# Performance work log

Hardware: AMD Instinct MI355X
Metric: run time of the kernel (lower is better)

Reference implementation:

```python
import jax, jax.numpy as jnp
import numpy as np

N_NODES = 50000
N_EDGES = 400000
N_GRAPHS = 64
EMB = 64
H = 128
EPS = 1e-5


def _prelu(x, a):
    return jnp.where(x > 0, x, a * x)


def _batchnorm(x, gamma, beta):
    mu = x.mean(0)
    var = x.var(0)
    return gamma * (x - mu) * jax.lax.rsqrt(var + EPS) + beta


def _sage_layer(xs, W_self, W_neigh, b, a, gamma, beta, src, dst):
    # xs: list of 3 [N, Din]; params stacked over the 3 relations
    outs = []
    for i in range(3):
        x = xs[i]
        msg = x[src[i]]                                   # [E, Din] neighbor gather
        nsum = jax.ops.segment_sum(msg, dst[i], num_segments=N_NODES)
        deg = jax.ops.segment_sum(jnp.ones((src.shape[1], 1), x.dtype), dst[i], num_segments=N_NODES)
        nmean = nsum / jnp.maximum(deg, 1.0)              # zero-degree -> 0 (DGL mean reduce)
        out = x @ W_self[i] + nmean @ W_neigh[i] + b[i]
        out = _prelu(out, a[i])                           # PReLU(h_feats)
        out = _batchnorm(out, gamma[i], beta[i])          # BatchNorm1d over nodes
        outs.append(out)
    return outs


def setup_inputs() -> dict:
    key = jax.random.key(0)
    ks = jax.random.split(key, 24)
    f32 = jnp.float32
    s = 0.05
    inp = {
        'h_idx': jax.random.randint(ks[0], (N_NODES,), 0, 257),
        'p_idx': jax.random.randint(ks[1], (N_NODES,), 0, 257),
        'hp_idx': jax.random.randint(ks[2], (N_NODES,), 0, 257),
        'src': jax.random.randint(ks[3], (3, N_EDGES), 0, N_NODES),
        'dst': jax.random.randint(ks[4], (3, N_EDGES), 0, N_NODES),
        'seg': jnp.sort(jax.random.randint(ks[5], (3, N_NODES), 0, N_GRAPHS), axis=1),
        'emb_h': jax.random.normal(ks[6], (257, EMB), f32) * s,
        'emb_p': jax.random.normal(ks[7], (257, EMB), f32) * s,
        'emb_hp': jax.random.normal(ks[8], (257, EMB), f32) * s,
        # layer 1 (in = EMB)
        'W1_self': jax.random.normal(ks[9], (3, EMB, H), f32) * s,
        'W1_neigh': jax.random.normal(ks[10], (3, EMB, H), f32) * s,
        'b1': jnp.zeros((3, H), f32),
        'a1': jnp.full((3, H), 0.25, f32),
        'gamma1': jnp.ones((3, H), f32),
        'beta1': jnp.zeros((3, H), f32),
        # layers 2-4 (in = H)
        'W_self': jax.random.normal(ks[11], (3, 3, H, H), f32) * s,
        'W_neigh': jax.random.normal(ks[12], (3, 3, H, H), f32) * s,
        'b': jnp.zeros((3, 3, H), f32),
        'a': jnp.full((3, 3, H), 0.25, f32),
        'gamma': jnp.ones((3, 3, H), f32),
        'beta': jnp.zeros((3, 3, H), f32),
    }
    return inp


def reference(h_idx, p_idx, hp_idx, src, dst, seg,
              emb_h, emb_p, emb_hp,
              W1_self, W1_neigh, b1, a1, gamma1, beta1,
              W_self, W_neigh, b, a, gamma, beta):
    xs = [emb_h[h_idx], emb_p[p_idx], emb_hp[hp_idx]]      # embedding lookups
    h1 = _sage_layer(xs, W1_self, W1_neigh, b1, a1, gamma1, beta1, src, dst)
    h2 = _sage_layer(h1, W_self[0], W_neigh[0], b[0], a[0], gamma[0], beta[0], src, dst)
    h3 = _sage_layer(h2, W_self[1], W_neigh[1], b[1], a[1], gamma[1], beta[1], src, dst)
    h4 = _sage_layer(h3, W_self[2], W_neigh[2], b[2], a[2], gamma[2], beta[2], src, dst)
    vecs = []
    for i in range(3):
        hcat = jnp.concatenate((h1[i], h2[i], h3[i], h4[i]), axis=1)   # [N, 4H]
        gsum = jax.ops.segment_sum(hcat, seg[i], num_segments=N_GRAPHS)
        cnt = jax.ops.segment_sum(jnp.ones((N_NODES, 1), hcat.dtype), seg[i], num_segments=N_GRAPHS)
        vecs.append(gsum / jnp.maximum(cnt, 1.0))                      # mean_nodes
    return jnp.concatenate(vecs, axis=1)                               # [B, 12H]
```

## Files before the change

kernel.cpp:

```cpp
#include <hip/hip_runtime.h>

#define N_NODES 50000
#define N_EDGES 400000
#define N_GRAPHS 64
#define EMB 64
#define H 128
#define EPS 1e-5f

#define NCHD 8
#define CHD 6250
#define NSLICE 48

typedef __attribute__((ext_vector_type(8))) short bf16x8;
typedef __attribute__((ext_vector_type(4))) float f32x4;

__device__ __forceinline__ unsigned short f2b(float f) {
    unsigned int u = __builtin_bit_cast(unsigned int, f);
    unsigned int r = (u + 0x7fff + ((u >> 16) & 1)) >> 16;
    return (unsigned short)r;
}


__global__ void count_deg_kernel(const int* __restrict__ dst, int* __restrict__ deg) {
    int rel = blockIdx.y;
    int e = blockIdx.x * 256 + threadIdx.x;
    if (e < N_EDGES) atomicAdd(&deg[rel * N_NODES + dst[rel * N_EDGES + e]], 1);
}

__global__ void scan_kernel(const int* __restrict__ deg, int* __restrict__ row_ptr,
                            int* __restrict__ cur) {
    int rel = blockIdx.x;
    const int* d = deg + rel * N_NODES;
    int* rp = row_ptr + rel * (N_NODES + 1);
    int* cu = cur + rel * N_NODES;
    __shared__ int sm[1024];
    __shared__ int carry;
    if (threadIdx.x == 0) carry = 0;
    __syncthreads();
    for (int base = 0; base < N_NODES; base += 4096) {
        int i0 = base + (int)threadIdx.x * 4;
        int v[4];
        int s = 0;
#pragma unroll
        for (int k = 0; k < 4; k++) { v[k] = (i0 + k < N_NODES) ? d[i0 + k] : 0; s += v[k]; }
        sm[threadIdx.x] = s;
        __syncthreads();
        for (int off = 1; off < 1024; off <<= 1) {
            int t = (threadIdx.x >= off) ? sm[threadIdx.x - off] : 0;
            __syncthreads();
            sm[threadIdx.x] += t;
            __syncthreads();
        }
        int run = carry + sm[threadIdx.x] - s;
#pragma unroll
        for (int k = 0; k < 4; k++) {
            if (i0 + k < N_NODES) { rp[i0 + k] = run; cu[i0 + k] = run; }
            run += v[k];
        }
        __syncthreads();
        if (threadIdx.x == 1023) carry += sm[1023];
        __syncthreads();
    }
    if (threadIdx.x == 0) rp[N_NODES] = carry;
}

__global__ void fill_part_kernel(const int* __restrict__ src, const int* __restrict__ dst,
                                 int* __restrict__ cur, int* __restrict__ edge_src) {
    int rel = blockIdx.z;
    int lo = blockIdx.y * CHD, hi = lo + CHD;
    const int* ds = dst + (size_t)rel * N_EDGES;
    const int* ss = src + (size_t)rel * N_EDGES;
    int* cu = cur + rel * N_NODES;
    int* es = edge_src + (size_t)rel * N_EDGES;
    for (int e = blockIdx.x * 256 + threadIdx.x; e < N_EDGES; e += NSLICE * 256) {
        int dn = ds[e];
        if (dn >= lo && dn < hi) {
            int pos = atomicAdd(&cu[dn], 1);
            es[pos] = ss[e];
        }
    }
}

__global__ void sort_adj_kernel(const int* __restrict__ row_ptr, int* __restrict__ edge_src) {
    int i = blockIdx.x * 256 + threadIdx.x;
    if (i >= 3 * N_NODES) return;
    int rel = i / N_NODES, n = i - rel * N_NODES;
    const int* rp = row_ptr + rel * (N_NODES + 1);
    int* es = edge_src + rel * N_EDGES;
    int s0 = rp[n], s1 = rp[n + 1];
    for (int a = s0 + 1; a < s1; a++) {
        int key = es[a];
        int b = a - 1;
        while (b >= s0 && es[b] > key) { es[b + 1] = es[b]; b--; }
        es[b + 1] = key;
    }
}


__global__ void prep_init_kernel(const float* __restrict__ W1self, const float* __restrict__ W1neigh,
                                 unsigned short* __restrict__ Wbt1,
                                 const float* __restrict__ emb_h, const float* __restrict__ emb_p,
                                 const float* __restrict__ emb_hp,
                                 unsigned short* __restrict__ emb_bf) {
    if (blockIdx.x < 192) {
        int idx = blockIdx.x * 256 + threadIdx.x;
        int rel = idx / (H * 128), rem = idx % (H * 128);
        int c = rem / 128, k = rem % 128;
        float v = (k < 64) ? W1self[((size_t)rel * 64 + k) * H + c]
                           : W1neigh[((size_t)rel * 64 + (k - 64)) * H + c];
        Wbt1[idx] = f2b(v);
    } else {
        int i = (blockIdx.x - 192) * 256 + threadIdx.x;
        if (i >= 3 * 257 * EMB / 8) return;
        int rel = i / (257 * EMB / 8), j = i % (257 * EMB / 8);
        const float* emb = rel == 0 ? emb_h : (rel == 1 ? emb_p : emb_hp);
        const float* e = emb + (size_t)j * 8;
        unsigned short o[8];
#pragma unroll
        for (int k = 0; k < 8; k++) o[k] = f2b(e[k]);
        *(uint4*)&emb_bf[(size_t)rel * 257 * EMB + (size_t)j * 8] = *(uint4*)o;
    }
}


__global__ __launch_bounds__(256) void aggregate1_kernel(
        const int* __restrict__ h_idx, const int* __restrict__ p_idx,
        const int* __restrict__ hp_idx,
        const unsigned short* __restrict__ emb_bf,
        const int* __restrict__ row_ptr, const int* __restrict__ edge_src,
        unsigned short* __restrict__ nmean) {
    const int TPN = 8;
    int rel = blockIdx.y;
    int node = blockIdx.x * 32 + threadIdx.x / TPN;
    int c8 = (threadIdx.x % TPN) * 8;
    if (node >= N_NODES) return;
    const int* idxarr = rel == 0 ? h_idx : (rel == 1 ? p_idx : hp_idx);
    const unsigned short* emb = emb_bf + (size_t)rel * 257 * EMB;
    const int* rp = row_ptr + rel * (N_NODES + 1);
    const int* es = edge_src + rel * N_EDGES;
    int s0 = rp[node], s1 = rp[node + 1];
    float acc[8];
#pragma unroll
    for (int j = 0; j < 8; j++) acc[j] = 0.f;

#define ACCUM(V)                                                                      \
    {                                                                                 \
        unsigned int w[4] = {(V).x, (V).y, (V).z, (V).w};                             \
        _Pragma("unroll") for (int j = 0; j < 4; j++) {                               \
            acc[2 * j] += __builtin_bit_cast(float, w[j] << 16);                      \
            acc[2 * j + 1] += __builtin_bit_cast(float, w[j] & 0xffff0000u);          \
        }                                                                             \
    }

    int e = s0;
    for (; e + 4 <= s1; e += 4) {
        int i0 = idxarr[es[e]], i1 = idxarr[es[e + 1]];
        int i2 = idxarr[es[e + 2]], i3 = idxarr[es[e + 3]];
        uint4 v0 = *(const uint4*)&emb[(size_t)i0 * EMB + c8];
        uint4 v1 = *(const uint4*)&emb[(size_t)i1 * EMB + c8];
        uint4 v2 = *(const uint4*)&emb[(size_t)i2 * EMB + c8];
        uint4 v3 = *(const uint4*)&emb[(size_t)i3 * EMB + c8];
        ACCUM(v0) ACCUM(v1) ACCUM(v2) ACCUM(v3)
    }
    for (; e < s1; e++) {
        uint4 v0 = *(const uint4*)&emb[(size_t)idxarr[es[e]] * EMB + c8];
        ACCUM(v0)
    }
    int deg = s1 - s0;
    float inv = 1.f / (float)max(deg, 1);
    unsigned short o[8];
#pragma unroll
    for (int j = 0; j < 8; j++)
        o[j] = (deg > 0) ? f2b(acc[j] * inv) : (unsigned short)0;
    *(uint4*)&nmean[((size_t)rel * N_NODES + node) * EMB + c8] = *(uint4*)o;
}


template <bool FOLD>
__global__ __launch_bounds__(256) void aggregate_kernel(
        const unsigned short* __restrict__ x,
        const int* __restrict__ row_ptr, const int* __restrict__ edge_src,
        const float* __restrict__ st,
        unsigned short* __restrict__ nmean) {
    const int TPN = 16;
    int rel = blockIdx.y;
    int c8 = (threadIdx.x % TPN) * 8;
    int nloc = threadIdx.x / TPN;
    const int* rp = row_ptr + rel * (N_NODES + 1);
    const int* es = edge_src + rel * N_EDGES;
    const unsigned short* xr = x + (size_t)rel * N_NODES * H;

    float sj[8], tj[8];
    if (FOLD) {
#pragma unroll
        for (int j = 0; j < 8; j++) {
            sj[j] = st[rel * 2 * H + c8 + j];
            tj[j] = st[rel * 2 * H + H + c8 + j];
        }
    }

#pragma unroll
    for (int batch = 0; batch < 6; batch++) {
        int node = blockIdx.x * 96 + batch * 16 + nloc;
        if (node >= N_NODES) continue;
        int s0 = rp[node], s1 = rp[node + 1];
        float acc[8];
#pragma unroll
        for (int j = 0; j < 8; j++) acc[j] = 0.f;
        int e = s0;
        for (; e + 4 <= s1; e += 4) {
            int i0 = es[e], i1 = es[e + 1], i2 = es[e + 2], i3 = es[e + 3];
            uint4 v0 = *(const uint4*)&xr[(size_t)i0 * H + c8];
            uint4 v1 = *(const uint4*)&xr[(size_t)i1 * H + c8];
            uint4 v2 = *(const uint4*)&xr[(size_t)i2 * H + c8];
            uint4 v3 = *(const uint4*)&xr[(size_t)i3 * H + c8];
            ACCUM(v0) ACCUM(v1) ACCUM(v2) ACCUM(v3)
        }
        for (; e < s1; e++) {
            uint4 v0 = *(const uint4*)&xr[(size_t)es[e] * H + c8];
            ACCUM(v0)
        }
        int deg = s1 - s0;
        float inv = 1.f / (float)max(deg, 1);
        unsigned short o[8];
#pragma unroll
        for (int j = 0; j < 8; j++) {
            float m = acc[j] * inv;
            if (FOLD) m = sj[j] * m + tj[j];
            o[j] = (deg > 0) ? f2b(m) : (unsigned short)0;
        }
        *(uint4*)&nmean[((size_t)rel * N_NODES + node) * H + c8] = *(uint4*)o;
    }
#undef ACCUM
}


template <int KX, bool G1>
__global__ __launch_bounds__(256) void gemm_kernel(
        const unsigned short* __restrict__ x,
        const unsigned short* __restrict__ nmean,
        const unsigned short* __restrict__ Wbt,
        const float* __restrict__ bias,
        const float* __restrict__ alpha,
        unsigned short* __restrict__ out,
        float* __restrict__ stats,
        const int* __restrict__ seg_all,
        float* __restrict__ gout,
        int layer,
        const unsigned short* __restrict__ embt,
        const int* __restrict__ h_idx, const int* __restrict__ p_idx,
        const int* __restrict__ hp_idx) {
    const int KTOT = 2 * KX;
    int rel = blockIdx.y;
    int row0 = blockIdx.x * 128;
    const unsigned short* xr = x + (size_t)rel * N_NODES * KX;
    const unsigned short* nm = nmean + (size_t)rel * N_NODES * KX;
    const unsigned short* W = Wbt + (size_t)rel * H * KTOT;
    unsigned short* o = out + (size_t)rel * N_NODES * H;

    __shared__ __align__(16) short At[128][40];
    __shared__ __align__(16) short Bt[128][40];

    int tid = threadIdx.x;
    int lane = tid & 63;
    int wave = tid >> 6;
    int wr = wave >> 1, wc = wave & 1;
    int l15 = lane & 15;
    int koff = (lane >> 4) * 8;

    f32x4 acc[4][4];
#pragma unroll
    for (int m = 0; m < 4; m++)
#pragma unroll
        for (int n = 0; n < 4; n++) acc[m][n] = (f32x4){0.f, 0.f, 0.f, 0.f};

    int seg = tid & 3;
    int rloc = tid >> 2;

    int nid0 = 0, nid1 = 0;
    if (G1) {
        const int* idxarr = rel == 0 ? h_idx : (rel == 1 ? p_idx : hp_idx);
        if (row0 + rloc < N_NODES) nid0 = idxarr[row0 + rloc];
        if (row0 + 64 + rloc < N_NODES) nid1 = idxarr[row0 + 64 + rloc];
    }
    const unsigned short* et = G1 ? (embt + (size_t)rel * 257 * EMB) : nullptr;

    for (int kc = 0; kc < KTOT; kc += 32) {
        const bool selfh = kc < KX;
        const unsigned short* Asrc = selfh ? xr : nm;
        int kb = selfh ? kc : kc - KX;
#pragma unroll
        for (int i = 0; i < 2; i++) {
            int r = i * 64 + rloc;
            int gr = row0 + r;
            uint4 v = make_uint4(0u, 0u, 0u, 0u);
            if (gr < N_NODES) {
                if (G1 && selfh) {
                    int nid = i ? nid1 : nid0;
                    v = *(const uint4*)&et[(size_t)nid * EMB + kb + seg * 8];
                } else {
                    v = *(const uint4*)&Asrc[(size_t)gr * KX + kb + seg * 8];
                }
            }
            *(uint4*)&At[r][seg * 8] = v;
        }
#pragma unroll
        for (int i = 0; i < 2; i++) {
            int c = i * 64 + rloc;
            *(uint4*)&Bt[c][seg * 8] = *(const uint4*)&W[(size_t)c * KTOT + kc + seg * 8];
        }
        __syncthreads();
        bf16x8 a[4], b[4];
#pragma unroll
        for (int m = 0; m < 4; m++) a[m] = *(const bf16x8*)&At[wr * 64 + m * 16 + l15][koff];
#pragma unroll
        for (int n = 0; n < 4; n++) b[n] = *(const bf16x8*)&Bt[wc * 64 + n * 16 + l15][koff];
#pragma unroll
        for (int m = 0; m < 4; m++)
#pragma unroll
            for (int n = 0; n < 4; n++)
                acc[m][n] = __builtin_amdgcn_mfma_f32_16x16x32_bf16(a[m], b[n], acc[m][n], 0, 0, 0);
        __syncthreads();
    }

    float bs[4], as_[4];
#pragma unroll
    for (int n = 0; n < 4; n++) {
        int col = wc * 64 + n * 16 + l15;
        bs[n] = bias[rel * H + col];
        as_[n] = alpha[rel * H + col];
    }
    const int* sg = seg_all + rel * N_NODES;
    float csum[4] = {0.f, 0.f, 0.f, 0.f}, cssq[4] = {0.f, 0.f, 0.f, 0.f};
    int curg = -1;
    float run[4] = {0.f, 0.f, 0.f, 0.f};
    int rbase = row0 + wr * 64 + (lane >> 4) * 4;
#pragma unroll
    for (int m = 0; m < 4; m++) {
#pragma unroll
        for (int j = 0; j < 4; j++) {
            int r = rbase + m * 16 + j;
            if (r >= N_NODES) continue;
            int g = sg[r];
            if (g != curg) {
                if (curg >= 0) {
                    float* ob = gout + (size_t)curg * (3 * 4 * H) + rel * (4 * H) + layer * H + wc * 64 + l15;
#pragma unroll
                    for (int n = 0; n < 4; n++) { atomicAdd(ob + n * 16, run[n]); run[n] = 0.f; }
                }
                curg = g;
            }
#pragma unroll
            for (int n = 0; n < 4; n++) {
                float v = acc[m][n][j] + bs[n];
                v = v > 0.f ? v : as_[n] * v;
                o[(size_t)r * H + wc * 64 + n * 16 + l15] = f2b(v);
                csum[n] += v;
                cssq[n] += v * v;
                run[n] += v;
            }
        }
    }
    if (curg >= 0) {
        float* ob = gout + (size_t)curg * (3 * 4 * H) + rel * (4 * H) + layer * H + wc * 64 + l15;
#pragma unroll
        for (int n = 0; n < 4; n++) atomicAdd(ob + n * 16, run[n]);
    }
    __syncthreads();
    float* smS = (float*)&At[0][0];
    float* smQ = (float*)&Bt[0][0];
    int contrib = wr * 4 + (lane >> 4);
#pragma unroll
    for (int n = 0; n < 4; n++) {
        int col = wc * 64 + n * 16 + l15;
        smS[col * 8 + contrib] = csum[n];
        smQ[col * 8 + contrib] = cssq[n];
    }
    __syncthreads();
    if (tid < 128) {
        float s = 0.f, q = 0.f;
#pragma unroll
        for (int i = 0; i < 8; i++) { s += smS[tid * 8 + i]; q += smQ[tid * 8 + i]; }
        atomicAdd(&stats[rel * 256 + tid], s);
        atomicAdd(&stats[rel * 256 + 128 + tid], q);
    }
}


__global__ void finalize_kernel(float* __restrict__ stats,
                                const float* __restrict__ gamma, const float* __restrict__ beta,
                                float* __restrict__ st) {
    int rel = blockIdx.x, c = threadIdx.x;
    const float invN = 1.f / N_NODES;
    float mu = stats[rel * 256 + c] * invN;
    float var = stats[rel * 256 + 128 + c] * invN - mu * mu;
    float s = gamma[rel * H + c] * rsqrtf(var + EPS);
    st[rel * 2 * H + c] = s;
    st[rel * 2 * H + H + c] = beta[rel * H + c] - mu * s;
    stats[rel * 256 + c] = 0.f;
    stats[rel * 256 + 128 + c] = 0.f;
}


__global__ void prep_kernel(const float* __restrict__ Wself, const float* __restrict__ Wneigh,
                            const float* __restrict__ b, const float* __restrict__ st,
                            unsigned short* __restrict__ Wbt, float* __restrict__ biasp) {
    if (blockIdx.x < 384) {
        int idx = blockIdx.x * 256 + threadIdx.x;
        int rel = idx / (H * 256), rem = idx % (H * 256);
        int c = rem / 256, k = rem % 256;
        float v;
        if (k < 128) v = st[rel * 2 * H + k] * Wself[((size_t)rel * H + k) * H + c];
        else         v = Wneigh[((size_t)rel * H + (k - 128)) * H + c];
        Wbt[idx] = f2b(v);
    } else if (threadIdx.x < H) {
        int rel = blockIdx.x - 384, c = threadIdx.x;
        const float* t = st + rel * 2 * H + H;
        float s = b[rel * H + c];
        for (int k = 0; k < H; k++) s += t[k] * Wself[((size_t)rel * H + k) * H + c];
        biasp[rel * H + c] = s;
    }
}


__global__ void scale_out_kernel(float* __restrict__ out, const int* __restrict__ seg,
                                 const float* __restrict__ st_all) {
    int i = blockIdx.x * 256 + threadIdx.x;
    if (i >= N_GRAPHS * 3 * 4 * H) return;
    int g = i / (3 * 4 * H), k = i % (3 * 4 * H);
    int rel = k / (4 * H), rem = k % (4 * H), layer = rem / H, c = rem % H;
    const int* sg = seg + rel * N_NODES;
    int lo = 0, hi = N_NODES;
    while (lo < hi) { int m = (lo + hi) >> 1; if (sg[m] < g) lo = m + 1; else hi = m; }
    int start = lo;
    hi = N_NODES;
    while (lo < hi) { int m = (lo + hi) >> 1; if (sg[m] <= g) lo = m + 1; else hi = m; }
    int cnt = lo - start;
    float mean = out[i] / (float)max(cnt, 1);
    const float* st = st_all + ((size_t)layer * 3 + rel) * 2 * H;
    out[i] = st[c] * mean + st[H + c];
}


extern "C" void kernel_launch(void* const* d_in, const int* in_sizes, int n_in,
                              void* d_out, int out_size, void* d_ws, size_t ws_size,
                              hipStream_t stream) {
    const int* h_idx = (const int*)d_in[0];
    const int* p_idx = (const int*)d_in[1];
    const int* hp_idx = (const int*)d_in[2];
    const int* src = (const int*)d_in[3];
    const int* dst = (const int*)d_in[4];
    const int* seg = (const int*)d_in[5];
    const float* emb_h = (const float*)d_in[6];
    const float* emb_p = (const float*)d_in[7];
    const float* emb_hp = (const float*)d_in[8];
    const float* W1_self = (const float*)d_in[9];
    const float* W1_neigh = (const float*)d_in[10];
    const float* b1 = (const float*)d_in[11];
    const float* a1 = (const float*)d_in[12];
    const float* gamma1 = (const float*)d_in[13];
    const float* beta1 = (const float*)d_in[14];
    const float* W_self = (const float*)d_in[15];
    const float* W_neigh = (const float*)d_in[16];
    const float* b = (const float*)d_in[17];
    const float* a = (const float*)d_in[18];
    const float* gamma = (const float*)d_in[19];
    const float* beta = (const float*)d_in[20];
    float* out = (float*)d_out;

    char* p = (char*)d_ws;
    unsigned short* hpA = (unsigned short*)p; p += (size_t)3 * N_NODES * H * 2;
    unsigned short* hpB = (unsigned short*)p; p += (size_t)3 * N_NODES * H * 2;
    unsigned short* Wbt1 = (unsigned short*)p; p += (size_t)3 * H * 128 * 2;
    unsigned short* Wbt = (unsigned short*)p; p += (size_t)3 * H * 256 * 2;
    unsigned short* emb_bf = (unsigned short*)p; p += (size_t)3 * 257 * EMB * 2;
    float* biasp = (float*)p; p += 3 * H * sizeof(float);
    float* st_all = (float*)p; p += 4 * 3 * 2 * H * sizeof(float);
    float* stats = (float*)p; p += 3 * 256 * sizeof(float);
    int* deg = (int*)p; p += (size_t)3 * N_NODES * 4;
    int* row_ptr = (int*)p; p += (size_t)3 * (N_NODES + 1) * 4;
    int* cur = (int*)p; p += (size_t)3 * N_NODES * 4;
    int* edge_src = (int*)p; p += (size_t)3 * N_EDGES * 4;

    hipMemsetAsync(out, 0, (size_t)N_GRAPHS * 3 * 4 * H * sizeof(float), stream);
    hipMemsetAsync(stats, 0, 3 * 256 * 4, stream);

    hipMemsetAsync(deg, 0, (size_t)3 * N_NODES * 4, stream);
    dim3 eb((N_EDGES + 255) / 256, 3);
    count_deg_kernel<<<eb, 256, 0, stream>>>(dst, deg);
    scan_kernel<<<3, 1024, 0, stream>>>(deg, row_ptr, cur);
    fill_part_kernel<<<dim3(NSLICE, NCHD, 3), 256, 0, stream>>>(src, dst, cur, edge_src);
    sort_adj_kernel<<<(3 * N_NODES + 255) / 256, 256, 0, stream>>>(row_ptr, edge_src);

    prep_init_kernel<<<217, 256, 0, stream>>>(W1_self, W1_neigh, Wbt1,
                                              emb_h, emb_p, emb_hp, emb_bf);

    dim3 gemm_grid((N_NODES + 127) / 128, 3);
    dim3 agg_grid((N_NODES + 95) / 96, 3);

    aggregate1_kernel<<<dim3((N_NODES + 31) / 32, 3), 256, 0, stream>>>(
        h_idx, p_idx, hp_idx, emb_bf, row_ptr, edge_src, hpB);
    gemm_kernel<64, true><<<gemm_grid, 256, 0, stream>>>(
        emb_bf , hpB, Wbt1, b1, a1, hpA, stats, seg, out, 0,
        emb_bf, h_idx, p_idx, hp_idx);
    finalize_kernel<<<3, H, 0, stream>>>(stats, gamma1, beta1, st_all);

    unsigned short* xin = hpA;
    unsigned short* xout = hpB;
    for (int l = 0; l < 3; l++) {
        const float* st_prev = st_all + (size_t)l * 3 * 2 * H;
        prep_kernel<<<387, 256, 0, stream>>>(
            W_self + (size_t)l * 3 * H * H, W_neigh + (size_t)l * 3 * H * H,
            b + (size_t)l * 3 * H, st_prev, Wbt, biasp);
        aggregate_kernel<true><<<agg_grid, 256, 0, stream>>>(
            xin, row_ptr, edge_src, st_prev, xout);
        gemm_kernel<128, false><<<gemm_grid, 256, 0, stream>>>(
            xin, xout, Wbt, biasp, a + (size_t)l * 3 * H, xout, stats, seg, out, l + 1,
            nullptr, nullptr, nullptr, nullptr);
        finalize_kernel<<<3, H, 0, stream>>>(
            stats, gamma + (size_t)l * 3 * H, beta + (size_t)l * 3 * H,
            st_all + (size_t)(l + 1) * 3 * 2 * H);
        unsigned short* t = xin; xin = xout; xout = t;
    }

    scale_out_kernel<<<(N_GRAPHS * 3 * 4 * H + 255) / 256, 256, 0, stream>>>(out, seg, st_all);
}
```

Measured before the change: 659.7 us.

## Replace chunk-filtered CSR fill with two-pass bucketed partition; skip final layer store

The old CSR fill had every block scan all edges and keep only those whose destination fell in its chunk, so the edge list was read eight times. It is replaced by a two-pass scheme. The first pass counts edges into 1024-node buckets in shared memory and scatters packed (src,dst) pairs into bucket-contiguous ranges, using per-bucket cursors seeded by the scan kernel. The second pass does the per-node atomic fill from the bucketed buffer. Separately, the last layer's GEMM no longer writes its unused node-feature output. This adds a 9.6MB scratch buffer and an extra kernel launch.

Measured after the change: 651.2 us. About the same (-1.3%).

```diff
diff --git a/kernel.cpp b/kernel.cpp
--- a/kernel.cpp
+++ b/kernel.cpp
@@ -7,9 +7,8 @@
 #define H 128
 #define EPS 1e-5f
 
-#define NCHD 8
-#define CHD 6250
-#define NSLICE 48
+#define NCH2 49
+#define NSLA 48
 
 typedef __attribute__((ext_vector_type(8))) short bf16x8;
 typedef __attribute__((ext_vector_type(4))) float f32x4;
@@ -28,7 +27,7 @@
 }
 
 __global__ void scan_kernel(const int* __restrict__ deg, int* __restrict__ row_ptr,
-                            int* __restrict__ cur) {
+                            int* __restrict__ cur, int* __restrict__ gcur) {
     int rel = blockIdx.x;
     const int* d = deg + rel * N_NODES;
     int* rp = row_ptr + rel * (N_NODES + 1);
@@ -54,7 +53,12 @@
         int run = carry + sm[threadIdx.x] - s;
 #pragma unroll
         for (int k = 0; k < 4; k++) {
-            if (i0 + k < N_NODES) { rp[i0 + k] = run; cu[i0 + k] = run; }
+            int i = i0 + k;
+            if (i < N_NODES) {
+                rp[i] = run;
+                cu[i] = run;
+                if ((i & 1023) == 0) gcur[rel * NCH2 + (i >> 10)] = run;
+            }
             run += v[k];
         }
         __syncthreads();
@@ -64,20 +68,48 @@
     if (threadIdx.x == 0) rp[N_NODES] = carry;
 }
 
-__global__ void fill_part_kernel(const int* __restrict__ src, const int* __restrict__ dst,
-                                 int* __restrict__ cur, int* __restrict__ edge_src) {
-    int rel = blockIdx.z;
-    int lo = blockIdx.y * CHD, hi = lo + CHD;
+__global__ __launch_bounds__(256) void partA_kernel(
+        const int* __restrict__ src, const int* __restrict__ dst,
+        int* __restrict__ gcur, unsigned long long* __restrict__ chunkbuf) {
+    int rel = blockIdx.y;
     const int* ds = dst + (size_t)rel * N_EDGES;
     const int* ss = src + (size_t)rel * N_EDGES;
+    unsigned long long* cb = chunkbuf + (size_t)rel * N_EDGES;
+    __shared__ int cnt[NCH2];
+    __shared__ int lcur[NCH2];
+    int tid = threadIdx.x;
+    if (tid < NCH2) cnt[tid] = 0;
+    __syncthreads();
+    for (int e = blockIdx.x * 256 + tid; e < N_EDGES; e += NSLA * 256)
+        atomicAdd(&cnt[ds[e] >> 10], 1);
+    __syncthreads();
+    if (tid < NCH2) lcur[tid] = atomicAdd(&gcur[rel * NCH2 + tid], cnt[tid]);
+    __syncthreads();
+    for (int e = blockIdx.x * 256 + tid; e < N_EDGES; e += NSLA * 256) {
+        int dn = ds[e], sn = ss[e];
+        int idx = atomicAdd(&lcur[dn >> 10], 1);
+        cb[idx] = ((unsigned long long)(unsigned)sn << 32) | (unsigned)dn;
+    }
+}
+
+__global__ __launch_bounds__(256) void fillB_kernel(
+        const int* __restrict__ row_ptr, const unsigned long long* __restrict__ chunkbuf,
+        int* __restrict__ cur, int* __restrict__ edge_src) {
+    int rel = blockIdx.y;
+    int c = blockIdx.x >> 1, half = blockIdx.x & 1;
+    const int* rp = row_ptr + rel * (N_NODES + 1);
+    int lo = rp[c << 10];
+    int hiN = min((c + 1) << 10, N_NODES);
+    int hi = rp[hiN];
+    const unsigned long long* cb = chunkbuf + (size_t)rel * N_EDGES;
     int* cu = cur + rel * N_NODES;
     int* es = edge_src + (size_t)rel * N_EDGES;
-    for (int e = blockIdx.x * 256 + threadIdx.x; e < N_EDGES; e += NSLICE * 256) {
-        int dn = ds[e];
-        if (dn >= lo && dn < hi) {
-            int pos = atomicAdd(&cu[dn], 1);
-            es[pos] = ss[e];
-        }
+    for (int i = lo + half + 2 * (int)threadIdx.x; i < hi; i += 2 * 256) {
+        unsigned long long pr = cb[i];
+        int dn = (int)(pr & 0xffffffffu);
+        int sn = (int)(pr >> 32);
+        int pos = atomicAdd(&cu[dn], 1);
+        es[pos] = sn;
     }
 }
 
@@ -235,7 +267,7 @@
 }
 
 
-template <int KX, bool G1>
+template <int KX, bool G1, bool STORE>
 __global__ __launch_bounds__(256) void gemm_kernel(
         const unsigned short* __restrict__ x,
         const unsigned short* __restrict__ nmean,
@@ -354,7 +386,7 @@
             for (int n = 0; n < 4; n++) {
                 float v = acc[m][n][j] + bs[n];
                 v = v > 0.f ? v : as_[n] * v;
-                o[(size_t)r * H + wc * 64 + n * 16 + l15] = f2b(v);
+                if (STORE) o[(size_t)r * H + wc * 64 + n * 16 + l15] = f2b(v);
                 csum[n] += v;
                 cssq[n] += v * v;
                 run[n] += v;
@@ -480,7 +512,9 @@
     int* deg = (int*)p; p += (size_t)3 * N_NODES * 4;
     int* row_ptr = (int*)p; p += (size_t)3 * (N_NODES + 1) * 4;
     int* cur = (int*)p; p += (size_t)3 * N_NODES * 4;
+    int* gcur = (int*)p; p += (size_t)3 * NCH2 * 4;
     int* edge_src = (int*)p; p += (size_t)3 * N_EDGES * 4;
+    unsigned long long* chunkbuf = (unsigned long long*)p; p += (size_t)3 * N_EDGES * 8;
 
     hipMemsetAsync(out, 0, (size_t)N_GRAPHS * 3 * 4 * H * sizeof(float), stream);
     hipMemsetAsync(stats, 0, 3 * 256 * 4, stream);
@@ -488,8 +522,9 @@
     hipMemsetAsync(deg, 0, (size_t)3 * N_NODES * 4, stream);
     dim3 eb((N_EDGES + 255) / 256, 3);
     count_deg_kernel<<<eb, 256, 0, stream>>>(dst, deg);
-    scan_kernel<<<3, 1024, 0, stream>>>(deg, row_ptr, cur);
-    fill_part_kernel<<<dim3(NSLICE, NCHD, 3), 256, 0, stream>>>(src, dst, cur, edge_src);
+    scan_kernel<<<3, 1024, 0, stream>>>(deg, row_ptr, cur, gcur);
+    partA_kernel<<<dim3(NSLA, 3), 256, 0, stream>>>(src, dst, gcur, chunkbuf);
+    fillB_kernel<<<dim3(2 * NCH2, 3), 256, 0, stream>>>(row_ptr, chunkbuf, cur, edge_src);
     sort_adj_kernel<<<(3 * N_NODES + 255) / 256, 256, 0, stream>>>(row_ptr, edge_src);
 
     prep_init_kernel<<<217, 256, 0, stream>>>(W1_self, W1_neigh, Wbt1,
@@ -500,7 +535,7 @@
 
     aggregate1_kernel<<<dim3((N_NODES + 31) / 32, 3), 256, 0, stream>>>(
         h_idx, p_idx, hp_idx, emb_bf, row_ptr, edge_src, hpB);
-    gemm_kernel<64, true><<<gemm_grid, 256, 0, stream>>>(
+    gemm_kernel<64, true, true><<<gemm_grid, 256, 0, stream>>>(
         emb_bf , hpB, Wbt1, b1, a1, hpA, stats, seg, out, 0,
         emb_bf, h_idx, p_idx, hp_idx);
     finalize_kernel<<<3, H, 0, stream>>>(stats, gamma1, beta1, st_all);
@@ -514,9 +549,14 @@
             b + (size_t)l * 3 * H, st_prev, Wbt, biasp);
         aggregate_kernel<true><<<agg_grid, 256, 0, stream>>>(
             xin, row_ptr, edge_src, st_prev, xout);
-        gemm_kernel<128, false><<<gemm_grid, 256, 0, stream>>>(
-            xin, xout, Wbt, biasp, a + (size_t)l * 3 * H, xout, stats, seg, out, l + 1,
-            nullptr, nullptr, nullptr, nullptr);
+        if (l < 2)
+            gemm_kernel<128, false, true><<<gemm_grid, 256, 0, stream>>>(
+                xin, xout, Wbt, biasp, a + (size_t)l * 3 * H, xout, stats, seg, out, l + 1,
+                nullptr, nullptr, nullptr, nullptr);
+        else
+            gemm_kernel<128, false, false><<<gemm_grid, 256, 0, stream>>>(
+                xin, xout, Wbt, biasp, a + (size_t)l * 3 * H, xout, stats, seg, out, l + 1,
+                nullptr, nullptr, nullptr, nullptr);
         finalize_kernel<<<3, H, 0, stream>>>(
             stats, gamma + (size_t)l * 3 * H, beta + (size_t)l * 3 * H,
             st_all + (size_t)(l + 1) * 3 * 2 * H);
```
